# Kernel tuning notes

Measured on AMD Instinct MI355X. Metric: run time of the kernel, lower is better.

## Reference

```python
import jax, jax.numpy as jnp
import numpy as np

EPS = 1e-5


def setup_inputs() -> dict:
    key = jax.random.key(0)
    ks = jax.random.split(key, 12)
    B, C, H, W = 1, 512, 64, 64
    d = C // 8
    inp = {
        "x": jax.random.normal(ks[0], (B, C, H, W), jnp.float32),
        "y": jax.random.normal(ks[1], (B, C, H, W), jnp.float32),
        "s_m": jax.random.uniform(ks[2], (H, W), jnp.float32),
        "q_m": jax.random.uniform(ks[3], (H, W), jnp.float32),
        "Wq": jax.random.normal(ks[4], (d, C), jnp.float32) * (1.0 / np.sqrt(C)),
        "bq": jnp.zeros((d,), jnp.float32),
        "Wk": jax.random.normal(ks[5], (d, C), jnp.float32) * (1.0 / np.sqrt(C)),
        "bk": jnp.zeros((d,), jnp.float32),
        "Wv": jax.random.normal(ks[6], (C, C), jnp.float32) * (1.0 / np.sqrt(C)),
        "bv": jnp.zeros((C,), jnp.float32),
        "W1": jax.random.normal(ks[7], (C, C), jnp.float32) * (1.0 / np.sqrt(C)),
        "b1": jnp.zeros((C,), jnp.float32),
        "W2": jax.random.normal(ks[8], (C, C), jnp.float32) * (1.0 / np.sqrt(C)),
        "b2": jnp.zeros((C,), jnp.float32),
        "gamma": jnp.ones((1, C, H, W), jnp.float32),
        "beta": jnp.zeros((1, C, H, W), jnp.float32),
    }
    return inp


def _conv1x1(x, Wt, b):
    # 1x1 Conv2d == per-pixel channel matmul
    return jnp.einsum("bchw,oc->bohw", x, Wt) + b[None, :, None, None]


def reference(x, y, s_m, q_m, Wq, bq, Wk, bk, Wv, bv, W1, b1, W2, b2, gamma, beta):
    B, C, H, W = x.shape
    N = H * W
    scale = (C // 8) ** (-0.5)

    q_m = jnp.where(q_m > 0.8, 1.0, 0.0).astype(x.dtype)
    x_fg = x * s_m[None, None]
    y_fg = y * q_m[None, None]

    def branch(q_in, k_in, v_in, use_max):
        q = _conv1x1(q_in, Wq, bq).reshape(B, -1, N).transpose(0, 2, 1) * scale  # [B,N,d]
        k = _conv1x1(k_in, Wk, bk).reshape(B, -1, N)                             # [B,d,N]
        v = _conv1x1(v_in, Wv, bv).reshape(B, -1, N)                             # [B,C,N]
        attn = jnp.einsum("bqd,bdk->bqk", q, k)                                  # [B,N,N]
        stat = jnp.max(attn) if use_max else jnp.min(attn)
        thr = (stat + jnp.mean(attn)) * 0.5
        attn = jnp.where(attn < thr, jnp.asarray(-999.0, attn.dtype), attn)
        attn = jax.nn.softmax(attn, axis=-1)
        out = jnp.einsum("bck,bqk->bcq", v, attn).reshape(B, C, H, W)
        h = out.transpose(0, 2, 3, 1)                                            # [B,H,W,C]
        h = jnp.maximum(h @ W1.T + b1, 0.0) @ W2.T + b2
        out = h.transpose(0, 3, 1, 2)
        # LayerNorm over all trailing dims [1,C,H,W] (B==1)
        mu = jnp.mean(out)
        var = jnp.mean((out - mu) ** 2)
        out = (out - mu) * jax.lax.rsqrt(var + EPS) * gamma + beta
        return out

    outx = branch(x_fg, y_fg, y_fg, True)
    outx = outx * s_m[None, None] + x * (1.0 - s_m)[None, None]
    outy = branch(y_fg, x, x, False)
    outy = outy * q_m[None, None] + y * (1.0 - q_m)[None, None]
    return outx, outy
```

## Files before the change

### kernel.cpp

```cpp
#include <hip/hip_runtime.h>
#include <math.h>

#define C_DIM 512
#define N_DIM 4096
#define CN (C_DIM * N_DIM)
#define SZO (N_DIM * C_DIM)
#define NN ((size_t)N_DIM * N_DIM)
#define NN_TOT ((long long)N_DIM * N_DIM)

typedef __attribute__((ext_vector_type(4))) float f32x4;
typedef __attribute__((ext_vector_type(8))) short short8;

__device__ __forceinline__ ushort f2bf(float f) {
    unsigned u = __float_as_uint(f);
    unsigned r = u + 0x7FFFu + ((u >> 16) & 1u);
    return (ushort)(r >> 16);
}
__device__ __forceinline__ float bf2f(ushort h) {
    return __uint_as_float((unsigned)h << 16);
}

__device__ __forceinline__ void gload16(const void* g, void* l) {
    __builtin_amdgcn_global_load_lds(
        (const __attribute__((address_space(1))) void*)g,
        (__attribute__((address_space(3))) void*)l, 16, 0, 0);
}

__global__ __launch_bounds__(256) void tconv64(
    const float* __restrict__ x, const float* __restrict__ y,
    ushort* __restrict__ xbT, ushort* __restrict__ ybT)
{
    const float* X = blockIdx.z ? y : x;
    ushort* XT = blockIdx.z ? ybT : xbT;
    __shared__ float t[64][65];
    const int c0 = blockIdx.x * 64;
    const int r0 = blockIdx.y * 64;
    const int ty = threadIdx.x >> 4, tx = threadIdx.x & 15;
    #pragma unroll
    for (int i = 0; i < 4; ++i) {
        int r = ty + i * 16;
        float4 v = *(const float4*)&X[(size_t)(r0 + r) * N_DIM + c0 + tx * 4];
        t[r][tx * 4 + 0] = v.x; t[r][tx * 4 + 1] = v.y;
        t[r][tx * 4 + 2] = v.z; t[r][tx * 4 + 3] = v.w;
    }
    __syncthreads();
    #pragma unroll
    for (int i = 0; i < 4; ++i) {
        int nn = ty + i * 16;
        ushort4 o;
        o.x = f2bf(t[tx * 4 + 0][nn]); o.y = f2bf(t[tx * 4 + 1][nn]);
        o.z = f2bf(t[tx * 4 + 2][nn]); o.w = f2bf(t[tx * 4 + 3][nn]);
        *(ushort4*)&XT[(size_t)(c0 + nn) * C_DIM + r0 + tx * 4] = o;
    }
}

__global__ __launch_bounds__(256) void cvtw3(
    const float* __restrict__ Wv, const float* __restrict__ W1,
    const float* __restrict__ W2, ushort* __restrict__ Wvb,
    ushort* __restrict__ W1b, ushort* __restrict__ W2b)
{
    const float* in  = (blockIdx.y == 0) ? Wv : (blockIdx.y == 1) ? W1 : W2;
    ushort*      out = (blockIdx.y == 0) ? Wvb : (blockIdx.y == 1) ? W1b : W2b;
    int i = (blockIdx.x * 256 + threadIdx.x) * 4;
    float4 v = *(const float4*)&in[i];
    ushort4 o = { f2bf(v.x), f2bf(v.y), f2bf(v.z), f2bf(v.w) };
    *(ushort4*)&out[i] = o;
}

template<int BM, int BN>
__global__ __launch_bounds__(256) void mfma_g(
    const ushort* __restrict__ A0, const ushort* __restrict__ A1,
    const ushort* __restrict__ B0, const ushort* __restrict__ B1,
    void* __restrict__ Out, size_t outBrStride,
    int M, int N, int K, int kLen, int nkz, int swapxy,
    const float* __restrict__ bias, int biasMode,
    const float* __restrict__ mask0, int mm0,
    const float* __restrict__ mask1, int mm1,
    int doRelu, int outBf16, float* __restrict__ lnp)
{
    constexpr int WAVES_M = BM / 64;
    constexpr int WAVES_N = 4 / WAVES_M;
    constexpr int WN = BN / WAVES_N;
    constexpr int FM = 4;
    constexpr int FN = WN / 16;
    constexpr int NCHUNK = (BM + BN) / 16;

    __shared__ ushort As[2][BM * 32];
    __shared__ ushort Bs[2][BN * 32];
    const int tid  = threadIdx.x;
    const int lane = tid & 63;
    const int wid  = tid >> 6;
    const int z  = blockIdx.z;
    const int br = z / nkz;
    const int kz = z % nkz;
    const ushort* A = br ? A1 : A0;
    const ushort* B = br ? B1 : B0;
    const float* mask = br ? mask1 : mask0;
    const int maskMode = br ? mm1 : mm0;

    const int bxm = swapxy ? blockIdx.x : blockIdx.y;
    const int bxn = swapxy ? blockIdx.y : blockIdx.x;
    const int m0 = bxm * BM, n0 = bxn * BN;
    const int wm = wid / WAVES_N, wn = wid % WAVES_N;
    const int wr = wm * 64, wc = wn * WN;
    const int kOff = kz * kLen;
    const int lrow = lane >> 2;
    const int kbl  = lane & 3;

    auto stage = [&](int buf, int t) {
        #pragma unroll
        for (int c = wid; c < NCHUNK; c += 4) {
            if (c < BM / 16) {
                int r = c * 16 + lrow;
                int kb = kbl ^ ((r >> 1) & 3);
                gload16(A + (size_t)(m0 + r) * K + kOff + t * 32 + kb * 8,
                        &As[buf][c * 512]);
            } else {
                int cb = c - BM / 16;
                int r = cb * 16 + lrow;
                int kb = kbl ^ ((r >> 1) & 3);
                gload16(B + (size_t)(n0 + r) * K + kOff + t * 32 + kb * 8,
                        &Bs[buf][cb * 512]);
            }
        }
    };

    f32x4 acc[FM][FN] = {};
    const int fr = lane & 15;
    const int kq = lane >> 4;
    const int nt = kLen / 32;

    stage(0, 0);
    asm volatile("s_waitcnt vmcnt(0)" ::: "memory");
    __syncthreads();
    int cur = 0;
    for (int t = 0; t < nt; ++t) {
        if (t + 1 < nt) stage(cur ^ 1, t + 1);
        short8 af[FM], bf[FN];
        #pragma unroll
        for (int mr = 0; mr < FM; ++mr) {
            int rA = wr + mr * 16 + fr;
            af[mr] = *(const short8*)&As[cur][rA * 32 + (kq ^ ((rA >> 1) & 3)) * 8];
        }
        #pragma unroll
        for (int nc = 0; nc < FN; ++nc) {
            int rB = wc + nc * 16 + fr;
            bf[nc] = *(const short8*)&Bs[cur][rB * 32 + (kq ^ ((rB >> 1) & 3)) * 8];
        }
        #pragma unroll
        for (int mr = 0; mr < FM; ++mr)
            #pragma unroll
            for (int nc = 0; nc < FN; ++nc)
                acc[mr][nc] = __builtin_amdgcn_mfma_f32_16x16x32_bf16(
                    af[mr], bf[nc], acc[mr][nc], 0, 0, 0);
        asm volatile("s_waitcnt vmcnt(0)" ::: "memory");
        __syncthreads();
        cur ^= 1;
    }

    const int orow = (lane >> 4) * 4;
    const int ocol = lane & 15;

    if (nkz > 1) {
        float* Of = (float*)Out + (size_t)z * M * N;
        #pragma unroll
        for (int mr = 0; mr < FM; ++mr)
            #pragma unroll
            for (int nc = 0; nc < FN; ++nc)
                #pragma unroll
                for (int j = 0; j < 4; ++j) {
                    int gm = m0 + wr + mr * 16 + orow + j;
                    int gn = n0 + wc + nc * 16 + ocol;
                    Of[(size_t)gm * N + gn] = acc[mr][nc][j];
                }
        return;
    }

    float mcol[FN], bcol[FN];
    #pragma unroll
    for (int nc = 0; nc < FN; ++nc) {
        int gn = n0 + wc + nc * 16 + ocol;
        mcol[nc] = (maskMode == 0) ? 1.0f
                 : (maskMode == 1) ? mask[gn]
                                   : (mask[gn] > 0.8f ? 1.0f : 0.0f);
        bcol[nc] = (biasMode == 2) ? bias[gn] : 0.0f;
    }
    ushort* Obf = (ushort*)Out + (size_t)br * outBrStride;
    float*  Of  = (float*)Out + (size_t)br * outBrStride;
    float lsum = 0.0f, lsq = 0.0f;
    #pragma unroll
    for (int mr = 0; mr < FM; ++mr) {
        #pragma unroll
        for (int j = 0; j < 4; ++j) {
            int gm = m0 + wr + mr * 16 + orow + j;
            float brow = (biasMode == 1) ? bias[gm] : 0.0f;
            #pragma unroll
            for (int nc = 0; nc < FN; ++nc) {
                int gn = n0 + wc + nc * 16 + ocol;
                float v = acc[mr][nc][j] * mcol[nc] + brow + bcol[nc];
                if (doRelu) v = fmaxf(v, 0.0f);
                if (outBf16) Obf[(size_t)gm * N + gn] = f2bf(v);
                else         Of[(size_t)gm * N + gn] = v;
                lsum += v; lsq = fmaf(v, v, lsq);
            }
        }
    }
    if (lnp) {
        __shared__ float redS[256], redQ[256];
        redS[tid] = lsum; redQ[tid] = lsq;
        __syncthreads();
        for (int s = 128; s > 0; s >>= 1) {
            if (tid < s) { redS[tid] += redS[tid + s]; redQ[tid] += redQ[tid + s]; }
            __syncthreads();
        }
        if (tid == 0) {
            int fb = blockIdx.y * gridDim.x + blockIdx.x;
            lnp[br * 512 + fb] = redS[0];
            lnp[br * 512 + 256 + fb] = redQ[0];
        }
    }
}

__global__ __launch_bounds__(256) void qkraw(
    const float* __restrict__ Wq, const float* __restrict__ Wk,
    const float* __restrict__ x, const float* __restrict__ y,
    float* __restrict__ PX)
{
    const int mt   = blockIdx.y & 1;
    const int srcT = blockIdx.y >> 1;
    const int kz   = blockIdx.z;
    const float* W = mt ? Wk : Wq;
    const float* X = srcT ? y : x;

    __shared__ float As[16][65];
    __shared__ float Bs[16][65];
    const int tid = threadIdx.x;
    const int n0 = blockIdx.x * 64;
    const int ty = tid >> 4, tx = tid & 15;
    float acc[4][4] = {};
    const int kbase = kz * 256;

    for (int k0 = kbase; k0 < kbase + 256; k0 += 16) {
        {
            int mm = tid >> 2, kq = (tid & 3) * 4;
            const float4 w4 = *(const float4*)&W[(size_t)mm * 512 + k0 + kq];
            As[kq + 0][mm] = w4.x; As[kq + 1][mm] = w4.y;
            As[kq + 2][mm] = w4.z; As[kq + 3][mm] = w4.w;
        }
        {
            int kk = tid >> 4, nq = (tid & 15) * 4;
            *(float4*)&Bs[kk][nq] = *(const float4*)&X[(size_t)(k0 + kk) * N_DIM + n0 + nq];
        }
        __syncthreads();
        #pragma unroll
        for (int kk = 0; kk < 16; ++kk) {
            float a[4], b[4];
            #pragma unroll
            for (int r = 0; r < 4; ++r) a[r] = As[kk][ty * 4 + r];
            #pragma unroll
            for (int c = 0; c < 4; ++c) b[c] = Bs[kk][tx * 4 + c];
            #pragma unroll
            for (int r = 0; r < 4; ++r)
                #pragma unroll
                for (int c = 0; c < 4; ++c)
                    acc[r][c] = fmaf(a[r], b[c], acc[r][c]);
        }
        __syncthreads();
    }
    float* dst = PX + ((size_t)(kz * 2 + srcT) * 128 + mt * 64) * N_DIM;
    #pragma unroll
    for (int r = 0; r < 4; ++r) {
        float4 o = make_float4(acc[r][0], acc[r][1], acc[r][2], acc[r][3]);
        *(float4*)&dst[(size_t)(ty * 4 + r) * N_DIM + n0 + tx * 4] = o;
    }
}

__global__ __launch_bounds__(256) void qkfinish(
    const float* __restrict__ PX,
    const float* __restrict__ s_m, const float* __restrict__ q_m,
    const float* __restrict__ bq, const float* __restrict__ bk,
    ushort* __restrict__ QF0, ushort* __restrict__ KF0,
    ushort* __restrict__ QF1, ushort* __restrict__ KF1)
{
    int gid = blockIdx.x * 256 + threadIdx.x;
    int lane = gid & 63;
    int rest = gid >> 6;
    int blk = rest & 255;
    int tensor = rest >> 8;
    int fr = lane & 15, quad = lane >> 4;
    int n = blk * 16 + fr;

    int srcT, rowbase, isQ;
    const float* bias;
    ushort* dst;
    float mv, scale;
    if (tensor == 0)      { srcT = 0; rowbase = 0;  isQ = 1; bias = bq; dst = QF0; scale = 0.125f; mv = s_m[n]; }
    else if (tensor == 1) { srcT = 1; rowbase = 64; isQ = 0; bias = bk; dst = KF0; scale = 1.0f;   mv = (q_m[n] > 0.8f) ? 1.0f : 0.0f; }
    else if (tensor == 2) { srcT = 1; rowbase = 0;  isQ = 1; bias = bq; dst = QF1; scale = 0.125f; mv = (q_m[n] > 0.8f) ? 1.0f : 0.0f; }
    else                  { srcT = 0; rowbase = 64; isQ = 0; bias = bk; dst = KF1; scale = 1.0f;   mv = 1.0f; }

    ushort hi0[8], lo0[8], hi1[8], lo1[8];
    #pragma unroll
    for (int j = 0; j < 8; ++j) {
        int d0 = quad * 8 + j, d1 = 32 + d0;
        float v0 = 0.0f, v1 = 0.0f;
        #pragma unroll
        for (int kz = 0; kz < 2; ++kz) {
            size_t base = ((size_t)(kz * 2 + srcT) * 128 + rowbase);
            v0 += PX[(base + d0) * N_DIM + n];
            v1 += PX[(base + d1) * N_DIM + n];
        }
        v0 = (v0 * mv + bias[d0]) * scale;
        v1 = (v1 * mv + bias[d1]) * scale;
        hi0[j] = f2bf(v0); lo0[j] = f2bf(v0 - bf2f(hi0[j]));
        hi1[j] = f2bf(v1); lo1[j] = f2bf(v1 - bf2f(hi1[j]));
    }
    auto wr8 = [&](int kstep, const ushort* v) {
        size_t base = ((size_t)(blk * 6 + kstep) * 64 + lane) * 8;
        *(ushort4*)&dst[base]     = *(const ushort4*)&v[0];
        *(ushort4*)&dst[base + 4] = *(const ushort4*)&v[4];
    };
    wr8(0, hi0); wr8(1, hi1);
    if (isQ) { wr8(2, hi0); wr8(3, hi1); wr8(4, lo0); wr8(5, lo1); }
    else     { wr8(2, lo0); wr8(3, lo1); wr8(4, hi0); wr8(5, hi1); }
}

__device__ __forceinline__ void scores_mfma(
    const ushort* __restrict__ QF, const ushort* __restrict__ KF,
    int m0, int n0, int wr, int wc, int lane, f32x4 acc[4][4])
{
    const int blkA0 = (m0 + wr) >> 4;
    const int blkB0 = (n0 + wc) >> 4;
    #pragma unroll
    for (int s = 0; s < 6; ++s) {
        short8 af[4], bf[4];
        #pragma unroll
        for (int mr = 0; mr < 4; ++mr)
            af[mr] = *(const short8*)&QF[((size_t)((blkA0 + mr) * 6 + s) * 64 + lane) * 8];
        #pragma unroll
        for (int nc = 0; nc < 4; ++nc)
            bf[nc] = *(const short8*)&KF[((size_t)((blkB0 + nc) * 6 + s) * 64 + lane) * 8];
        #pragma unroll
        for (int mr = 0; mr < 4; ++mr)
            #pragma unroll
            for (int nc = 0; nc < 4; ++nc)
                acc[mr][nc] = __builtin_amdgcn_mfma_f32_16x16x32_bf16(
                    af[mr], bf[nc], acc[mr][nc], 0, 0, 0);
    }
}

__global__ __launch_bounds__(256) void scores_pass1(
    const ushort* __restrict__ QF0, const ushort* __restrict__ KF0,
    const ushort* __restrict__ QF1, const ushort* __restrict__ KF1,
    float* __restrict__ part, float* __restrict__ rowmaxp)
{
    const int br = blockIdx.z;
    const ushort* QF = br ? QF1 : QF0;
    const ushort* KF = br ? KF1 : KF0;
    part    += (size_t)br * 3072;
    rowmaxp += (size_t)br * 131072;

    const int lane = threadIdx.x & 63, wid = threadIdx.x >> 6;
    const int m0 = blockIdx.y * 128, n0 = blockIdx.x * 128;
    const int wr = (wid >> 1) * 64, wc = (wid & 1) * 64;
    f32x4 acc[4][4] = {};
    scores_mfma(QF, KF, m0, n0, wr, wc, lane, acc);

    float lmax = -3.4e38f, lmin = 3.4e38f, lsum = 0.0f;
    float rmx[4][4];
    #pragma unroll
    for (int mr = 0; mr < 4; ++mr)
        #pragma unroll
        for (int j = 0; j < 4; ++j) rmx[mr][j] = -3.4e38f;
    #pragma unroll
    for (int mr = 0; mr < 4; ++mr)
        #pragma unroll
        for (int nc = 0; nc < 4; ++nc)
            #pragma unroll
            for (int j = 0; j < 4; ++j) {
                float v = acc[mr][nc][j];
                lsum += v; lmax = fmaxf(lmax, v); lmin = fminf(lmin, v);
                rmx[mr][j] = fmaxf(rmx[mr][j], v);
            }
    #pragma unroll
    for (int m = 1; m < 16; m <<= 1)
        #pragma unroll
        for (int mr = 0; mr < 4; ++mr)
            #pragma unroll
            for (int j = 0; j < 4; ++j)
                rmx[mr][j] = fmaxf(rmx[mr][j], __shfl_xor(rmx[mr][j], m, 64));

    __shared__ float wrm[2][128];
    const int orow = (lane >> 4) * 4;
    if ((lane & 15) == 0) {
        #pragma unroll
        for (int mr = 0; mr < 4; ++mr)
            #pragma unroll
            for (int j = 0; j < 4; ++j)
                wrm[wid & 1][wr + mr * 16 + orow + j] = rmx[mr][j];
    }
    __syncthreads();
    if (threadIdx.x < 128) {
        float v = fmaxf(wrm[0][threadIdx.x], wrm[1][threadIdx.x]);
        rowmaxp[(size_t)blockIdx.x * 4096 + m0 + threadIdx.x] = v;
    }

    __shared__ float red[256];
    const int tid = threadIdx.x;
    const int bid = blockIdx.y * 32 + blockIdx.x;
    __syncthreads();
    red[tid] = lmax; __syncthreads();
    for (int s = 128; s > 0; s >>= 1) { if (tid < s) red[tid] = fmaxf(red[tid], red[tid + s]); __syncthreads(); }
    if (tid == 0) part[bid] = red[0];
    __syncthreads();
    red[tid] = lmin; __syncthreads();
    for (int s = 128; s > 0; s >>= 1) { if (tid < s) red[tid] = fminf(red[tid], red[tid + s]); __syncthreads(); }
    if (tid == 0) part[1024 + bid] = red[0];
    __syncthreads();
    red[tid] = lsum; __syncthreads();
    for (int s = 128; s > 0; s >>= 1) { if (tid < s) red[tid] += red[tid + s]; __syncthreads(); }
    if (tid == 0) part[2048 + bid] = red[0];
}

__global__ __launch_bounds__(256) void stats_fin2(
    const float* __restrict__ part, float* __restrict__ stats)
{
    const int br = blockIdx.x;
    part += (size_t)br * 3072;
    __shared__ float rmax[256], rmin[256];
    __shared__ double rsum[256];
    int tid = threadIdx.x;
    float m1 = -3.4e38f, m2 = 3.4e38f; double s = 0.0;
    for (int i = tid; i < 1024; i += 256) {
        m1 = fmaxf(m1, part[i]);
        m2 = fminf(m2, part[1024 + i]);
        s += (double)part[2048 + i];
    }
    rmax[tid] = m1; rmin[tid] = m2; rsum[tid] = s;
    __syncthreads();
    for (int st = 128; st > 0; st >>= 1) {
        if (tid < st) {
            rmax[tid] = fmaxf(rmax[tid], rmax[tid + st]);
            rmin[tid] = fminf(rmin[tid], rmin[tid + st]);
            rsum[tid] += rsum[tid + st];
        }
        __syncthreads();
    }
    if (tid == 0) {
        float stat = (br == 0) ? rmax[0] : rmin[0];
        float mean = (float)(rsum[0] / (double)NN_TOT);
        stats[br] = 0.5f * (stat + mean);
    }
}

__global__ __launch_bounds__(256) void row_fin(
    const float* __restrict__ rowmaxp, const float* __restrict__ stats,
    float* __restrict__ rowm)
{
    const int br = blockIdx.y;
    int r = blockIdx.x * 256 + threadIdx.x;
    float thr = stats[br];
    float m = -3.4e38f;
    #pragma unroll 8
    for (int b = 0; b < 32; ++b)
        m = fmaxf(m, rowmaxp[(size_t)br * 131072 + (size_t)b * 4096 + r]);
    rowm[br * 4096 + r] = (m >= thr) ? m : -1e30f;
}

__global__ __launch_bounds__(256) void scores_pass2(
    const ushort* __restrict__ QF0, const ushort* __restrict__ KF0,
    const ushort* __restrict__ QF1, const ushort* __restrict__ KF1,
    const float* __restrict__ stats, const float* __restrict__ rowm,
    ushort* __restrict__ Pe, float* __restrict__ rowsump)
{
    const int br = blockIdx.z;
    const ushort* QF = br ? QF1 : QF0;
    const ushort* KF = br ? KF1 : KF0;
    ushort* P = Pe + (size_t)br * NN;
    rowsump += (size_t)br * 131072;
    rowm    += (size_t)br * 4096;

    const int lane = threadIdx.x & 63, wid = threadIdx.x >> 6;
    const int m0 = blockIdx.y * 128, n0 = blockIdx.x * 128;
    const int wr = (wid >> 1) * 64, wc = (wid & 1) * 64;
    f32x4 acc[4][4] = {};
    scores_mfma(QF, KF, m0, n0, wr, wc, lane, acc);

    const float thr = stats[br];
    const int orow = (lane >> 4) * 4;
    const int ocol = lane & 15;
    float rm[4][4], rs[4][4];
    #pragma unroll
    for (int mr = 0; mr < 4; ++mr)
        #pragma unroll
        for (int j = 0; j < 4; ++j) {
            rm[mr][j] = rowm[m0 + wr + mr * 16 + orow + j];
            rs[mr][j] = 0.0f;
        }
    #pragma unroll
    for (int mr = 0; mr < 4; ++mr)
        #pragma unroll
        for (int nc = 0; nc < 4; ++nc)
            #pragma unroll
            for (int j = 0; j < 4; ++j) {
                float s = acc[mr][nc][j];
                float m = rm[mr][j];
                float e = (s < thr) ? 0.0f : __expf(s - m);
                if (m < -1e29f) e = 1.0f;
                ushort h = f2bf(e);
                rs[mr][j] += bf2f(h);
                P[(size_t)(m0 + wr + mr * 16 + orow + j) * N_DIM
                  + n0 + wc + nc * 16 + ocol] = h;
            }
    #pragma unroll
    for (int m = 1; m < 16; m <<= 1)
        #pragma unroll
        for (int mr = 0; mr < 4; ++mr)
            #pragma unroll
            for (int j = 0; j < 4; ++j)
                rs[mr][j] += __shfl_xor(rs[mr][j], m, 64);

    __shared__ float wrs[2][128];
    if ((lane & 15) == 0) {
        #pragma unroll
        for (int mr = 0; mr < 4; ++mr)
            #pragma unroll
            for (int j = 0; j < 4; ++j)
                wrs[wid & 1][wr + mr * 16 + orow + j] = rs[mr][j];
    }
    __syncthreads();
    if (threadIdx.x < 128)
        rowsump[(size_t)blockIdx.x * 4096 + m0 + threadIdx.x] =
            wrs[0][threadIdx.x] + wrs[1][threadIdx.x];
}

__global__ __launch_bounds__(256) void rsum_fin(
    const float* __restrict__ rowsump, float* __restrict__ invr)
{
    const int br = blockIdx.y;
    int r = blockIdx.x * 256 + threadIdx.x;
    float s = 0.0f;
    #pragma unroll 8
    for (int b = 0; b < 32; ++b)
        s += rowsump[(size_t)br * 131072 + (size_t)b * 4096 + r];
    invr[br * 4096 + r] = 1.0f / s;
}

__global__ __launch_bounds__(256) void reduce2row(
    const float* __restrict__ P4, const float* __restrict__ invr,
    ushort* __restrict__ O)
{
    const int br = blockIdx.y;
    int i = (blockIdx.x * 256 + threadIdx.x) * 4;
    int row = i >> 9;
    float sc = invr[br * 4096 + row];
    float4 a = *(const float4*)&P4[(size_t)(br * 2 + 0) * SZO + i];
    float4 b = *(const float4*)&P4[(size_t)(br * 2 + 1) * SZO + i];
    ushort4 o;
    o.x = f2bf((a.x + b.x) * sc);
    o.y = f2bf((a.y + b.y) * sc);
    o.z = f2bf((a.z + b.z) * sc);
    o.w = f2bf((a.w + b.w) * sc);
    *(ushort4*)&O[(size_t)br * SZO + i] = o;
}

__global__ __launch_bounds__(256) void ln_fin(
    const float* __restrict__ lnp, float* __restrict__ stats)
{
    const int br = blockIdx.x;
    const float* part = lnp + (size_t)br * 512;
    __shared__ double rs[256], rq[256];
    int tid = threadIdx.x;
    rs[tid] = (double)part[tid];
    rq[tid] = (double)part[256 + tid];
    __syncthreads();
    for (int st = 128; st > 0; st >>= 1) {
        if (tid < st) { rs[tid] += rs[tid + st]; rq[tid] += rq[tid + st]; }
        __syncthreads();
    }
    if (tid == 0) {
        double mu = rs[0] / (double)CN;
        double var = rq[0] / (double)CN - mu * mu;
        stats[4 + 2 * br] = (float)mu;
        stats[5 + 2 * br] = (float)(1.0 / sqrt(var + 1e-5));
    }
}

__global__ __launch_bounds__(256) void gate_write(
    const float* __restrict__ H2, const float* __restrict__ stats,
    const float* __restrict__ gamma, const float* __restrict__ beta,
    const float* __restrict__ x, const float* __restrict__ y,
    const float* __restrict__ s_m, const float* __restrict__ q_m,
    float* __restrict__ out)
{
    const int br = blockIdx.y;
    size_t i = ((size_t)blockIdx.x * 256 + threadIdx.x) * 4;
    int n = (int)(i & (N_DIM - 1));
    float mu = stats[4 + 2 * br], rstd = stats[5 + 2 * br];
    float4 h = *(const float4*)&H2[(size_t)br * CN + i];
    float4 g = *(const float4*)&gamma[i];
    float4 b = *(const float4*)&beta[i];
    const float* resid = br ? y : x;
    float4 r = *(const float4*)&resid[i];
    float4 o;
    float vals[4] = { h.x, h.y, h.z, h.w };
    float gs[4] = { g.x, g.y, g.z, g.w };
    float bs[4] = { b.x, b.y, b.z, b.w };
    float rs[4] = { r.x, r.y, r.z, r.w };
    float os[4];
    #pragma unroll
    for (int j = 0; j < 4; ++j) {
        float mv = br ? ((q_m[n + j] > 0.8f) ? 1.0f : 0.0f) : s_m[n + j];
        float normed = (vals[j] - mu) * rstd * gs[j] + bs[j];
        os[j] = normed * mv + rs[j] * (1.0f - mv);
    }
    o.x = os[0]; o.y = os[1]; o.z = os[2]; o.w = os[3];
    *(float4*)&out[(size_t)br * CN + i] = o;
}

extern "C" void kernel_launch(void* const* d_in, const int* in_sizes, int n_in,
                              void* d_out, int out_size, void* d_ws, size_t ws_size,
                              hipStream_t stream)
{
    const float* x     = (const float*)d_in[0];
    const float* y     = (const float*)d_in[1];
    const float* s_m   = (const float*)d_in[2];
    const float* q_m   = (const float*)d_in[3];
    const float* Wq    = (const float*)d_in[4];
    const float* bq    = (const float*)d_in[5];
    const float* Wk    = (const float*)d_in[6];
    const float* bk    = (const float*)d_in[7];
    const float* Wv    = (const float*)d_in[8];
    const float* bv    = (const float*)d_in[9];
    const float* W1    = (const float*)d_in[10];
    const float* b1    = (const float*)d_in[11];
    const float* W2    = (const float*)d_in[12];
    const float* b2    = (const float*)d_in[13];
    const float* gamma = (const float*)d_in[14];
    const float* beta  = (const float*)d_in[15];
    float* out = (float*)d_out;

    float* ws = (float*)d_ws;
    float*  R1    = ws;
    float*  PX    = R1;
    float*  P4    = R1;
    ushort* QF0   = (ushort*)(R1 + 4194304);
    ushort* KF0   = QF0 + 786432;
    ushort* QF1   = KF0 + 786432;
    ushort* KF1   = QF1 + 786432;
    float*  SMALL = R1 + 8388608;
    float*  PART  = SMALL;
    float*  RMAXP = PART + 6144;
    float*  RSUMP = RMAXP + 262144;
    float*  ROWM  = RSUMP + 262144;
    float*  INVR  = ROWM + 8192;
    float*  LNP   = INVR + 8192;
    float*  STATS = LNP + 1024;
    ushort* Wvb   = (ushort*)(STATS + 64);
    ushort* W1b   = Wvb + 262144;
    ushort* W2b   = W1b + 262144;
    ushort* Vb    = W2b + 262144;
    ushort* R2    = Vb + 4194304;
    ushort* xbT   = R2;
    ushort* ybT   = R2 + 2097152;
    ushort* Pe    = R2;
    ushort* O1T   = R2;
    ushort* H1T   = R2 + 4194304;
    float*  H2    = (float*)(R2 + 8388608);

    tconv64<<<dim3(64, 8, 2), 256, 0, stream>>>(x, y, xbT, ybT);
    cvtw3<<<dim3(256, 3), 256, 0, stream>>>(Wv, W1, W2, Wvb, W1b, W2b);

    qkraw<<<dim3(64, 4, 2), 256, 0, stream>>>(Wq, Wk, x, y, PX);
    qkfinish<<<256, 256, 0, stream>>>(PX, s_m, q_m, bq, bk, QF0, KF0, QF1, KF1);

    mfma_g<128, 128><<<dim3(32, 4, 2), 256, 0, stream>>>(
        Wvb, Wvb, ybT, xbT, Vb, (size_t)CN,
        512, 4096, 512, 512, 1, 0, bv, 1, q_m, 2, nullptr, 0, 0, 1, nullptr);

    scores_pass1<<<dim3(32, 32, 2), 256, 0, stream>>>(QF0, KF0, QF1, KF1, PART, RMAXP);
    stats_fin2<<<2, 256, 0, stream>>>(PART, STATS);
    row_fin<<<dim3(16, 2), 256, 0, stream>>>(RMAXP, STATS, ROWM);
    scores_pass2<<<dim3(32, 32, 2), 256, 0, stream>>>(QF0, KF0, QF1, KF1, STATS, ROWM, Pe, RSUMP);
    rsum_fin<<<dim3(16, 2), 256, 0, stream>>>(RSUMP, INVR);

    mfma_g<128, 128><<<dim3(32, 4, 4), 256, 0, stream>>>(
        Pe, Pe + NN, Vb, Vb + CN, P4, 0,
        4096, 512, 4096, 2048, 2, 1, nullptr, 0, nullptr, 0, nullptr, 0, 0, 0, nullptr);
    reduce2row<<<dim3(2048, 2), 256, 0, stream>>>(P4, INVR, O1T);

    mfma_g<128, 64><<<dim3(32, 8, 2), 256, 0, stream>>>(
        O1T, O1T + SZO, W1b, W1b, H1T, (size_t)SZO,
        4096, 512, 512, 512, 1, 1, b1, 2, nullptr, 0, nullptr, 0, 1, 1, nullptr);

    mfma_g<64, 128><<<dim3(32, 8, 2), 256, 0, stream>>>(
        W2b, W2b, H1T, H1T + SZO, H2, (size_t)CN,
        512, 4096, 512, 512, 1, 0, b2, 1, nullptr, 0, nullptr, 0, 0, 0, LNP);

    ln_fin<<<2, 256, 0, stream>>>(LNP, STATS);
    gate_write<<<dim3(2048, 2), 256, 0, stream>>>(
        H2, STATS, gamma, beta, x, y, s_m, q_m, out);
}
```

Measured before the change: 240.5 us.

## Fold tiny reduction kernels into consumers and shrink GEMM tiles for more blocks

Removes the row_fin, rsum_fin and ln_fin launches. Each block now recomputes its own row max, row sum inverse, or LayerNorm statistics from the partial buffers inside scores_pass2, reduce2row and gate_write. Separately, the V, PV and W1 GEMMs switch to smaller tile templates with twice as many blocks, to raise occupancy across the CUs. The cost is redundant reduction work in every block (gate_write repeats a 256-element double-precision reduction in each of its 4096 blocks) and less data reuse per tile.

```diff
diff --git a/kernel.cpp b/kernel.cpp
--- a/kernel.cpp
+++ b/kernel.cpp
@@ -453,24 +453,10 @@
     }
 }
 
-__global__ __launch_bounds__(256) void row_fin(
-    const float* __restrict__ rowmaxp, const float* __restrict__ stats,
-    float* __restrict__ rowm)
-{
-    const int br = blockIdx.y;
-    int r = blockIdx.x * 256 + threadIdx.x;
-    float thr = stats[br];
-    float m = -3.4e38f;
-    #pragma unroll 8
-    for (int b = 0; b < 32; ++b)
-        m = fmaxf(m, rowmaxp[(size_t)br * 131072 + (size_t)b * 4096 + r]);
-    rowm[br * 4096 + r] = (m >= thr) ? m : -1e30f;
-}
-
 __global__ __launch_bounds__(256) void scores_pass2(
     const ushort* __restrict__ QF0, const ushort* __restrict__ KF0,
     const ushort* __restrict__ QF1, const ushort* __restrict__ KF1,
-    const float* __restrict__ stats, const float* __restrict__ rowm,
+    const float* __restrict__ stats, const float* __restrict__ rowmaxp,
     ushort* __restrict__ Pe, float* __restrict__ rowsump)
 {
     const int br = blockIdx.z;
@@ -478,15 +464,27 @@
     const ushort* KF = br ? KF1 : KF0;
     ushort* P = Pe + (size_t)br * NN;
     rowsump += (size_t)br * 131072;
-    rowm    += (size_t)br * 4096;
+    rowmaxp += (size_t)br * 131072;
 
     const int lane = threadIdx.x & 63, wid = threadIdx.x >> 6;
     const int m0 = blockIdx.y * 128, n0 = blockIdx.x * 128;
     const int wr = (wid >> 1) * 64, wc = (wid & 1) * 64;
+    const float thr = stats[br];
+
+    __shared__ float rowmL[128];
+    if (threadIdx.x < 128) {
+        int r = m0 + threadIdx.x;
+        float m = -3.4e38f;
+        #pragma unroll 8
+        for (int b = 0; b < 32; ++b)
+            m = fmaxf(m, rowmaxp[(size_t)b * 4096 + r]);
+        rowmL[threadIdx.x] = (m >= thr) ? m : -1e30f;
+    }
+    __syncthreads();
+
     f32x4 acc[4][4] = {};
     scores_mfma(QF, KF, m0, n0, wr, wc, lane, acc);
 
-    const float thr = stats[br];
     const int orow = (lane >> 4) * 4;
     const int ocol = lane & 15;
     float rm[4][4], rs[4][4];
@@ -494,7 +492,7 @@
     for (int mr = 0; mr < 4; ++mr)
         #pragma unroll
         for (int j = 0; j < 4; ++j) {
-            rm[mr][j] = rowm[m0 + wr + mr * 16 + orow + j];
+            rm[mr][j] = rowmL[wr + mr * 16 + orow + j];
             rs[mr][j] = 0.0f;
         }
     #pragma unroll
@@ -534,26 +532,24 @@
             wrs[0][threadIdx.x] + wrs[1][threadIdx.x];
 }
 
-__global__ __launch_bounds__(256) void rsum_fin(
-    const float* __restrict__ rowsump, float* __restrict__ invr)
+__global__ __launch_bounds__(256) void reduce2row(
+    const float* __restrict__ P4, const float* __restrict__ rowsump,
+    ushort* __restrict__ O)
 {
     const int br = blockIdx.y;
-    int r = blockIdx.x * 256 + threadIdx.x;
-    float s = 0.0f;
-    #pragma unroll 8
-    for (int b = 0; b < 32; ++b)
-        s += rowsump[(size_t)br * 131072 + (size_t)b * 4096 + r];
-    invr[br * 4096 + r] = 1.0f / s;
-}
-
-__global__ __launch_bounds__(256) void reduce2row(
-    const float* __restrict__ P4, const float* __restrict__ invr,
-    ushort* __restrict__ O)
-{
-    const int br = blockIdx.y;
-    int i = (blockIdx.x * 256 + threadIdx.x) * 4;
-    int row = i >> 9;
-    float sc = invr[br * 4096 + row];
+    const int tid = threadIdx.x;
+    const int r0 = blockIdx.x * 2;
+    __shared__ float invL[2];
+    if (tid < 64) {
+        int rw = tid >> 5, b = tid & 31;
+        float s = rowsump[(size_t)br * 131072 + (size_t)b * 4096 + r0 + rw];
+        #pragma unroll
+        for (int m = 1; m < 32; m <<= 1) s += __shfl_xor(s, m, 64);
+        if (b == 0) invL[rw] = 1.0f / s;
+    }
+    __syncthreads();
+    int i = (blockIdx.x * 256 + tid) * 4;
+    float sc = invL[(i >> 9) & 1];
     float4 a = *(const float4*)&P4[(size_t)(br * 2 + 0) * SZO + i];
     float4 b = *(const float4*)&P4[(size_t)(br * 2 + 1) * SZO + i];
     ushort4 o;
@@ -564,57 +560,47 @@
     *(ushort4*)&O[(size_t)br * SZO + i] = o;
 }
 
-__global__ __launch_bounds__(256) void ln_fin(
-    const float* __restrict__ lnp, float* __restrict__ stats)
-{
-    const int br = blockIdx.x;
-    const float* part = lnp + (size_t)br * 512;
-    __shared__ double rs[256], rq[256];
-    int tid = threadIdx.x;
-    rs[tid] = (double)part[tid];
-    rq[tid] = (double)part[256 + tid];
-    __syncthreads();
-    for (int st = 128; st > 0; st >>= 1) {
-        if (tid < st) { rs[tid] += rs[tid + st]; rq[tid] += rq[tid + st]; }
-        __syncthreads();
-    }
-    if (tid == 0) {
-        double mu = rs[0] / (double)CN;
-        double var = rq[0] / (double)CN - mu * mu;
-        stats[4 + 2 * br] = (float)mu;
-        stats[5 + 2 * br] = (float)(1.0 / sqrt(var + 1e-5));
-    }
-}
-
 __global__ __launch_bounds__(256) void gate_write(
-    const float* __restrict__ H2, const float* __restrict__ stats,
+    const float* __restrict__ H2, const float* __restrict__ lnp,
     const float* __restrict__ gamma, const float* __restrict__ beta,
     const float* __restrict__ x, const float* __restrict__ y,
     const float* __restrict__ s_m, const float* __restrict__ q_m,
     float* __restrict__ out)
 {
     const int br = blockIdx.y;
-    size_t i = ((size_t)blockIdx.x * 256 + threadIdx.x) * 4;
+    const int tid = threadIdx.x;
+    __shared__ double rs[256], rq[256];
+    rs[tid] = (double)lnp[(size_t)br * 512 + tid];
+    rq[tid] = (double)lnp[(size_t)br * 512 + 256 + tid];
+    __syncthreads();
+    for (int st = 128; st > 0; st >>= 1) {
+        if (tid < st) { rs[tid] += rs[tid + st]; rq[tid] += rq[tid + st]; }
+        __syncthreads();
+    }
+    double muD = rs[0] / (double)CN;
+    double varD = rq[0] / (double)CN - muD * muD;
+    float mu = (float)muD;
+    float rstd = (float)(1.0 / sqrt(varD + 1e-5));
+
+    size_t i = ((size_t)blockIdx.x * 256 + tid) * 4;
     int n = (int)(i & (N_DIM - 1));
-    float mu = stats[4 + 2 * br], rstd = stats[5 + 2 * br];
     float4 h = *(const float4*)&H2[(size_t)br * CN + i];
     float4 g = *(const float4*)&gamma[i];
     float4 b = *(const float4*)&beta[i];
     const float* resid = br ? y : x;
     float4 r = *(const float4*)&resid[i];
-    float4 o;
     float vals[4] = { h.x, h.y, h.z, h.w };
     float gs[4] = { g.x, g.y, g.z, g.w };
     float bs[4] = { b.x, b.y, b.z, b.w };
-    float rs[4] = { r.x, r.y, r.z, r.w };
+    float rsv[4] = { r.x, r.y, r.z, r.w };
     float os[4];
     #pragma unroll
     for (int j = 0; j < 4; ++j) {
         float mv = br ? ((q_m[n + j] > 0.8f) ? 1.0f : 0.0f) : s_m[n + j];
         float normed = (vals[j] - mu) * rstd * gs[j] + bs[j];
-        os[j] = normed * mv + rs[j] * (1.0f - mv);
-    }
-    o.x = os[0]; o.y = os[1]; o.z = os[2]; o.w = os[3];
+        os[j] = normed * mv + rsv[j] * (1.0f - mv);
+    }
+    float4 o; o.x = os[0]; o.y = os[1]; o.z = os[2]; o.w = os[3];
     *(float4*)&out[(size_t)br * CN + i] = o;
 }
 
@@ -652,9 +638,7 @@
     float*  PART  = SMALL;
     float*  RMAXP = PART + 6144;
     float*  RSUMP = RMAXP + 262144;
-    float*  ROWM  = RSUMP + 262144;
-    float*  INVR  = ROWM + 8192;
-    float*  LNP   = INVR + 8192;
+    float*  LNP   = RSUMP + 262144;
     float*  STATS = LNP + 1024;
     ushort* Wvb   = (ushort*)(STATS + 64);
     ushort* W1b   = Wvb + 262144;
@@ -674,22 +658,20 @@
     qkraw<<<dim3(64, 4, 2), 256, 0, stream>>>(Wq, Wk, x, y, PX);
     qkfinish<<<256, 256, 0, stream>>>(PX, s_m, q_m, bq, bk, QF0, KF0, QF1, KF1);
 
-    mfma_g<128, 128><<<dim3(32, 4, 2), 256, 0, stream>>>(
+    mfma_g<64, 128><<<dim3(32, 8, 2), 256, 0, stream>>>(
         Wvb, Wvb, ybT, xbT, Vb, (size_t)CN,
         512, 4096, 512, 512, 1, 0, bv, 1, q_m, 2, nullptr, 0, 0, 1, nullptr);
 
     scores_pass1<<<dim3(32, 32, 2), 256, 0, stream>>>(QF0, KF0, QF1, KF1, PART, RMAXP);
     stats_fin2<<<2, 256, 0, stream>>>(PART, STATS);
-    row_fin<<<dim3(16, 2), 256, 0, stream>>>(RMAXP, STATS, ROWM);
-    scores_pass2<<<dim3(32, 32, 2), 256, 0, stream>>>(QF0, KF0, QF1, KF1, STATS, ROWM, Pe, RSUMP);
-    rsum_fin<<<dim3(16, 2), 256, 0, stream>>>(RSUMP, INVR);
-
-    mfma_g<128, 128><<<dim3(32, 4, 4), 256, 0, stream>>>(
+    scores_pass2<<<dim3(32, 32, 2), 256, 0, stream>>>(QF0, KF0, QF1, KF1, STATS, RMAXP, Pe, RSUMP);
+
+    mfma_g<64, 128><<<dim3(64, 4, 4), 256, 0, stream>>>(
         Pe, Pe + NN, Vb, Vb + CN, P4, 0,
         4096, 512, 4096, 2048, 2, 1, nullptr, 0, nullptr, 0, nullptr, 0, 0, 0, nullptr);
-    reduce2row<<<dim3(2048, 2), 256, 0, stream>>>(P4, INVR, O1T);
-
-    mfma_g<128, 64><<<dim3(32, 8, 2), 256, 0, stream>>>(
+    reduce2row<<<dim3(2048, 2), 256, 0, stream>>>(P4, RSUMP, O1T);
+
+    mfma_g<64, 64><<<dim3(64, 8, 2), 256, 0, stream>>>(
         O1T, O1T + SZO, W1b, W1b, H1T, (size_t)SZO,
         4096, 512, 512, 512, 1, 1, b1, 2, nullptr, 0, nullptr, 0, 1, 1, nullptr);
 
@@ -697,7 +679,6 @@
         W2b, W2b, H1T, H1T + SZO, H2, (size_t)CN,
         512, 4096, 512, 512, 1, 0, b2, 1, nullptr, 0, nullptr, 0, 0, 0, LNP);
 
-    ln_fin<<<2, 256, 0, stream>>>(LNP, STATS);
     gate_write<<<dim3(2048, 2), 256, 0, stream>>>(
-        H2, STATS, gamma, beta, x, y, s_m, q_m, out);
-}
+        H2, LNP, gamma, beta, x, y, s_m, q_m, out);
+}
```

New measurement: 255.9 us. +6.4%, slower.
